# Performance work log

Measured on AMD Instinct MI355X. Metric: run time of the kernel, lower is better.

Reference implementation:

```python
import jax, jax.numpy as jnp
import numpy as np

N, D, H, L, E, G, C = 50000, 128, 128, 5, 800000, 512, 10


def setup_inputs() -> dict:
    key = jax.random.key(0)
    ks = jax.random.split(key, 16)
    s = 0.1  # normal init std (Weight_Initializer == 3 style; any init is fine for a math baseline)
    return {
        "x": jax.random.normal(ks[0], (N, D), jnp.float32),
        "edge_index": jax.random.randint(ks[1], (2, E), 0, N, jnp.int32),
        "edge_mask": jax.random.uniform(ks[2], (E,), jnp.float32),
        "batch": jnp.sort(jax.random.randint(ks[3], (N,), 0, G, jnp.int32)),
        "num_graphs": G,
        "eps": jnp.zeros((L,), jnp.float32),
        # per-GIN-layer 2-layer MLP (num_slp_layers=2): D -> H -> D, weights stored [in, out]
        "mlp_w1": jax.random.normal(ks[4], (L, D, H), jnp.float32) * s,
        "mlp_b1": jnp.zeros((L, H), jnp.float32),
        "mlp_w2": jax.random.normal(ks[5], (L, H, D), jnp.float32) * s,
        "mlp_b2": jnp.zeros((L, D), jnp.float32),
        # classifier head: lin1 [(L+1)*D -> (L+1)*D], lin2 [(L+1)*D -> C]
        "lin1_w": jax.random.normal(ks[6], ((L + 1) * D, (L + 1) * D), jnp.float32) * s,
        "lin1_b": jnp.zeros(((L + 1) * D,), jnp.float32),
        "lin2_w": jax.random.normal(ks[7], ((L + 1) * D, C), jnp.float32) * s,
        "lin2_b": jnp.zeros((C,), jnp.float32),
    }


def reference(x, edge_index, edge_mask, batch, num_graphs, eps,
              mlp_w1, mlp_b1, mlp_w2, mlp_b2, lin1_w, lin1_b, lin2_w, lin2_b):
    n = x.shape[0]
    src, dst = edge_index[0], edge_index[1]
    embeds = [x]
    h = x
    for l in range(eps.shape[0]):
        # A @ h with A[src,dst] = edge_mask: gather neighbor feats, weight, scatter-add to src
        agg = jax.ops.segment_sum(edge_mask[:, None] * h[dst], src, num_segments=n)  # [N,D]
        pooled = agg + (1.0 + eps[l]) * h
        h1 = jax.nn.relu(pooled @ mlp_w1[l] + mlp_b1[l])
        h = jax.nn.relu(h1 @ mlp_w2[l] + mlp_b2[l])
        embeds.append(h)
    stacked = jnp.stack(embeds)  # [L+1, N, D]
    # global_add_pool per layer, then per-graph concat across layers -> [G, (L+1)*D]
    pooled_g = jax.vmap(lambda e: jax.ops.segment_sum(e, batch, num_segments=num_graphs))(stacked)
    merged = jnp.transpose(pooled_g, (1, 0, 2)).reshape(num_graphs, -1)
    lin1_out = jax.nn.relu(merged @ lin1_w + lin1_b)  # dropout p=0 -> identity
    lin2_out = lin1_out @ lin2_w + lin2_b
    return jax.nn.softmax(lin2_out, axis=1)  # [G, C]
```

## Files before the change

### kernel.cpp

```cpp
#include <hip/hip_runtime.h>


typedef __bf16 bf16x8 __attribute__((ext_vector_type(8)));
typedef float f32x4 __attribute__((ext_vector_type(4)));

static inline int ceil_div(int a, int b) { return (a + b - 1) / b; }

__device__ inline ushort bf_rne(float v) {
  unsigned u = __float_as_uint(v);
  return (ushort)((u + 0x7fffu + ((u >> 16) & 1u)) >> 16);
}
__device__ inline float bf2f(ushort u) { return __uint_as_float((unsigned)u << 16); }
__device__ inline float bf2f_lo(unsigned g) { return __uint_as_float(g << 16); }
__device__ inline float bf2f_hi(unsigned g) { return __uint_as_float(g & 0xffff0000u); }

__global__ void k_hist(const int* __restrict__ src, int* __restrict__ deg, int E) {
  int i = blockIdx.x * blockDim.x + threadIdx.x;
  if (i < E) atomicAdd(&deg[src[i]], 1);
}

__global__ __launch_bounds__(256) void k_scan1(const int* __restrict__ deg,
                                               int* __restrict__ excl,
                                               int* __restrict__ bsum, int N) {
  __shared__ int tsum[256];
  int b = blockIdx.x, t = threadIdx.x;
  int base = b * 1024 + t * 4;
  int v0 = 0, v1 = 0, v2 = 0, v3 = 0;
  if (base + 3 < N) {
    int4 q = *(const int4*)&deg[base];
    v0 = q.x; v1 = q.y; v2 = q.z; v3 = q.w;
  } else {
    if (base + 0 < N) v0 = deg[base + 0];
    if (base + 1 < N) v1 = deg[base + 1];
    if (base + 2 < N) v2 = deg[base + 2];
    if (base + 3 < N) v3 = deg[base + 3];
  }
  tsum[t] = v0 + v1 + v2 + v3;
  __syncthreads();
  for (int off = 1; off < 256; off <<= 1) {
    int x = (t >= off) ? tsum[t - off] : 0;
    __syncthreads();
    tsum[t] += x;
    __syncthreads();
  }
  int pre = (t == 0) ? 0 : tsum[t - 1];
  if (base < N)     excl[base]     = pre;
  if (base + 1 < N) excl[base + 1] = pre + v0;
  if (base + 2 < N) excl[base + 2] = pre + v0 + v1;
  if (base + 3 < N) excl[base + 3] = pre + v0 + v1 + v2;
  if (t == 255) bsum[b] = tsum[255];
}

__global__ __launch_bounds__(256) void k_scan2(const int* __restrict__ bsum,
                                               int* __restrict__ boff, int nb,
                                               int* __restrict__ rowptr_last) {
  __shared__ int s[256];
  int t = threadIdx.x;
  s[t] = (t < nb) ? bsum[t] : 0;
  __syncthreads();
  for (int off = 1; off < 256; off <<= 1) {
    int x = (t >= off) ? s[t - off] : 0;
    __syncthreads();
    s[t] += x;
    __syncthreads();
  }
  if (t < nb) boff[t] = (t == 0) ? 0 : s[t - 1];
  if (t == 255) *rowptr_last = s[255];
}

__global__ __launch_bounds__(256) void k_scan3(const int* __restrict__ excl,
                                               const int* __restrict__ boff,
                                               int* __restrict__ rowptr,
                                               int* __restrict__ cursor, int N) {
  int i = blockIdx.x * 256 + threadIdx.x;
  if (i < N) {
    int v = excl[i] + boff[i >> 10];
    rowptr[i] = v;
    cursor[i] = v;
  }
}

__global__ void k_scatter(const int* __restrict__ src, const int* __restrict__ dst,
                          const float* __restrict__ mask, int* __restrict__ cursor,
                          int2* __restrict__ sedge, int E) {
  int i = blockIdx.x * blockDim.x + threadIdx.x;
  if (i < E) {
    int s = src[i];
    int p = atomicAdd(&cursor[s], 1);
    sedge[p] = make_int2(dst[i], __float_as_int(mask[i]));
  }
}

__global__ __launch_bounds__(256) void k_tobf16(const float* __restrict__ in,
                                                ushort* __restrict__ out, int n) {
  int base = (blockIdx.x * 256 + threadIdx.x) * 4;
  if (base + 3 < n) {
    float4 v = *(const float4*)&in[base];
    ushort4 o;
    o.x = bf_rne(v.x); o.y = bf_rne(v.y); o.z = bf_rne(v.z); o.w = bf_rne(v.w);
    *(ushort4*)&out[base] = o;
  } else {
    for (int k = base; k < n; ++k) out[k] = bf_rne(in[k]);
  }
}

__global__ __launch_bounds__(256) void k_prepw(const float* __restrict__ W,
                                               ushort* __restrict__ hi,
                                               ushort* __restrict__ lo,
                                               int K, int N) {
  __shared__ float t[32][33];
  int mat = blockIdx.z;
  const float* Wm = W + (size_t)mat * K * N;
  ushort* him = hi + (size_t)mat * K * N;
  ushort* lom = lo + (size_t)mat * K * N;
  int k0 = blockIdx.x * 32, n0 = blockIdx.y * 32;
  int tx = threadIdx.x & 31, ty = threadIdx.x >> 5;
#pragma unroll
  for (int r = 0; r < 32; r += 8)
    t[ty + r][tx] = Wm[(size_t)(k0 + ty + r) * N + n0 + tx];
  __syncthreads();
#pragma unroll
  for (int r = 0; r < 32; r += 8) {
    float v = t[tx][ty + r];
    size_t o = (size_t)(n0 + ty + r) * K + k0 + tx;
    ushort h = bf_rne(v);
    him[o] = h;
    lom[o] = bf_rne(v - bf2f(h));
  }
}

__global__ __launch_bounds__(128) void k_agg(const ushort* __restrict__ h,
                                             const int* __restrict__ rowptr,
                                             const int2* __restrict__ sedge,
                                             const float* __restrict__ eps, int layer,
                                             ushort* __restrict__ pooled, int N) {
  int v = blockIdx.x * 2 + (threadIdx.x >> 6);
  int lane = threadIdx.x & 63;
  if (v >= N) return;
  int beg = rowptr[v], end = rowptr[v + 1];
  float ax[8] = {}, ay[8] = {};
  int j = beg;
  for (; j + 8 <= end; j += 8) {
    int2 e[8];
    unsigned g[8];
#pragma unroll
    for (int q = 0; q < 8; ++q) e[q] = sedge[j + q];
#pragma unroll
    for (int q = 0; q < 8; ++q)
      g[q] = *(const unsigned*)&h[(size_t)e[q].x * 128 + lane * 2];
#pragma unroll
    for (int q = 0; q < 8; ++q) {
      float m = __int_as_float(e[q].y);
      ax[q] = fmaf(m, bf2f_lo(g[q]), ax[q]);
      ay[q] = fmaf(m, bf2f_hi(g[q]), ay[q]);
    }
  }
  for (; j + 2 <= end; j += 2) {
    int2 e0 = sedge[j], e1 = sedge[j + 1];
    unsigned g0 = *(const unsigned*)&h[(size_t)e0.x * 128 + lane * 2];
    unsigned g1 = *(const unsigned*)&h[(size_t)e1.x * 128 + lane * 2];
    ax[0] = fmaf(__int_as_float(e0.y), bf2f_lo(g0), ax[0]);
    ay[0] = fmaf(__int_as_float(e0.y), bf2f_hi(g0), ay[0]);
    ax[1] = fmaf(__int_as_float(e1.y), bf2f_lo(g1), ax[1]);
    ay[1] = fmaf(__int_as_float(e1.y), bf2f_hi(g1), ay[1]);
  }
  if (j < end) {
    int2 e = sedge[j];
    unsigned g = *(const unsigned*)&h[(size_t)e.x * 128 + lane * 2];
    float m = __int_as_float(e.y);
    ax[0] = fmaf(m, bf2f_lo(g), ax[0]);
    ay[0] = fmaf(m, bf2f_hi(g), ay[0]);
  }
  float sx = ((ax[0] + ax[1]) + (ax[2] + ax[3])) + ((ax[4] + ax[5]) + (ax[6] + ax[7]));
  float sy = ((ay[0] + ay[1]) + (ay[2] + ay[3])) + ((ay[4] + ay[5]) + (ay[6] + ay[7]));
  float ep = 1.0f + eps[layer];
  unsigned gs = *(const unsigned*)&h[(size_t)v * 128 + lane * 2];
  sx = fmaf(ep, bf2f_lo(gs), sx);
  sy = fmaf(ep, bf2f_hi(gs), sy);
  unsigned outw = (unsigned)bf_rne(sx) | ((unsigned)bf_rne(sy) << 16);
  *(unsigned*)&pooled[(size_t)v * 128 + lane * 2] = outw;
}

__global__ __launch_bounds__(256) void k_mlp(
    const ushort* __restrict__ pooled,
    const ushort* __restrict__ w1t, const float* __restrict__ b1,
    const ushort* __restrict__ w2t, const float* __restrict__ b2,
    ushort* __restrict__ hout, int N) {
  __shared__ ushort As[64][128];
  __shared__ ushort Ws[128][128];
  __shared__ ushort H1s[64][128];
  int tid = threadIdx.x;
  int w = tid >> 6, lane = tid & 63;
  int row0 = blockIdx.x * 64;
  int wr = w >> 1, wc = w & 1;

#pragma unroll
  for (int i = 0; i < 4; ++i) {
    int f = i * 256 + tid;
    int r = f >> 4, c8 = (f & 15) * 8;
    int ksw = c8 ^ ((r & 7) << 3);
    if (row0 + r < N) {
      *(bf16x8*)&As[r][ksw] = *(const bf16x8*)&pooled[(size_t)(row0 + r) * 128 + c8];
    } else {
      ushort4 z = {0, 0, 0, 0};
      *(ushort4*)&As[r][ksw] = z;
      *(ushort4*)&As[r][ksw + 4] = z;
    }
  }
#pragma unroll
  for (int i = 0; i < 8; ++i) {
    int f = i * 256 + tid;
    int r = f >> 4, c8 = (f & 15) * 8;
    *(bf16x8*)&Ws[r][c8 ^ ((r & 7) << 3)] = *(const bf16x8*)&w1t[(size_t)r * 128 + c8];
  }
  __syncthreads();

  f32x4 acc[2][4];
#pragma unroll
  for (int m = 0; m < 2; ++m)
#pragma unroll
    for (int n = 0; n < 4; ++n) acc[m][n] = (f32x4){0.f, 0.f, 0.f, 0.f};
#pragma unroll
  for (int ks = 0; ks < 4; ++ks) {
    int kk = ks * 32 + (lane >> 4) * 8;
    bf16x8 a[2], b[4];
#pragma unroll
    for (int m = 0; m < 2; ++m) {
      int r = wr * 32 + m * 16 + (lane & 15);
      a[m] = *(bf16x8*)&As[r][kk ^ ((r & 7) << 3)];
    }
#pragma unroll
    for (int n = 0; n < 4; ++n) {
      int r = wc * 64 + n * 16 + (lane & 15);
      b[n] = *(bf16x8*)&Ws[r][kk ^ ((r & 7) << 3)];
    }
#pragma unroll
    for (int m = 0; m < 2; ++m)
#pragma unroll
      for (int n = 0; n < 4; ++n)
        acc[m][n] = __builtin_amdgcn_mfma_f32_16x16x32_bf16(a[m], b[n], acc[m][n], 0, 0, 0);
  }
#pragma unroll
  for (int m = 0; m < 2; ++m) {
    int rbase = wr * 32 + m * 16 + (lane >> 4) * 4;
#pragma unroll
    for (int n = 0; n < 4; ++n) {
      int col = wc * 64 + n * 16 + (lane & 15);
      float bb = b1[col];
#pragma unroll
      for (int r = 0; r < 4; ++r) {
        int row = rbase + r;
        float v = fmaxf(acc[m][n][r] + bb, 0.f);
        H1s[row][col ^ ((row & 7) << 3)] = bf_rne(v);
      }
    }
  }
  __syncthreads();

#pragma unroll
  for (int i = 0; i < 8; ++i) {
    int f = i * 256 + tid;
    int r = f >> 4, c8 = (f & 15) * 8;
    *(bf16x8*)&Ws[r][c8 ^ ((r & 7) << 3)] = *(const bf16x8*)&w2t[(size_t)r * 128 + c8];
  }
  __syncthreads();

#pragma unroll
  for (int m = 0; m < 2; ++m)
#pragma unroll
    for (int n = 0; n < 4; ++n) acc[m][n] = (f32x4){0.f, 0.f, 0.f, 0.f};
#pragma unroll
  for (int ks = 0; ks < 4; ++ks) {
    int kk = ks * 32 + (lane >> 4) * 8;
    bf16x8 a[2], b[4];
#pragma unroll
    for (int m = 0; m < 2; ++m) {
      int r = wr * 32 + m * 16 + (lane & 15);
      a[m] = *(bf16x8*)&H1s[r][kk ^ ((r & 7) << 3)];
    }
#pragma unroll
    for (int n = 0; n < 4; ++n) {
      int r = wc * 64 + n * 16 + (lane & 15);
      b[n] = *(bf16x8*)&Ws[r][kk ^ ((r & 7) << 3)];
    }
#pragma unroll
    for (int m = 0; m < 2; ++m)
#pragma unroll
      for (int n = 0; n < 4; ++n)
        acc[m][n] = __builtin_amdgcn_mfma_f32_16x16x32_bf16(a[m], b[n], acc[m][n], 0, 0, 0);
  }
#pragma unroll
  for (int m = 0; m < 2; ++m) {
    int rbase = row0 + wr * 32 + m * 16 + (lane >> 4) * 4;
#pragma unroll
    for (int n = 0; n < 4; ++n) {
      int col = wc * 64 + n * 16 + (lane & 15);
      float bb = b2[col];
#pragma unroll
      for (int r = 0; r < 4; ++r) {
        int row = rbase + r;
        if (row < N) {
          float v = fmaxf(acc[m][n][r] + bb, 0.f);
          hout[(size_t)row * 128 + col] = bf_rne(v);
        }
      }
    }
  }
}

template <int RELU, int OUT_BF16, int SPLITW>
__global__ __launch_bounds__(256) void k_mgemm(const ushort* __restrict__ A,
                                               const ushort* __restrict__ Wt_hi,
                                               const ushort* __restrict__ Wt_lo,
                                               const float* __restrict__ bias,
                                               void* __restrict__ Cout,
                                               int M, int N, int K) {
  __shared__ ushort As[64][128];
  __shared__ ushort Ws_hi[64][128];
  __shared__ ushort Ws_lo[SPLITW ? 64 : 1][SPLITW ? 128 : 1];
  int tid = threadIdx.x;
  int row0 = blockIdx.y * 64, col0 = blockIdx.x * 64;
  int w = tid >> 6, lane = tid & 63;
  int wr = w >> 1, wc = w & 1;
  f32x4 acc[2][2] = {};
  int nk = K >> 7;
  for (int kc = 0; kc < nk; ++kc) {
    int k0 = kc << 7;
    if (kc) __syncthreads();
#pragma unroll
    for (int i = 0; i < 4; ++i) {
      int f = i * 256 + tid;
      int r = f >> 4, c8 = (f & 15) * 8;
      int ksw = c8 ^ ((r & 7) << 3);
      if (row0 + r < M) {
        *(bf16x8*)&As[r][ksw] = *(const bf16x8*)&A[(size_t)(row0 + r) * K + k0 + c8];
      } else {
        ushort4 z = {0, 0, 0, 0};
        *(ushort4*)&As[r][ksw] = z;
        *(ushort4*)&As[r][ksw + 4] = z;
      }
    }
#pragma unroll
    for (int i = 0; i < 4; ++i) {
      int f = i * 256 + tid;
      int r = f >> 4, c8 = (f & 15) * 8;
      int ksw = c8 ^ ((r & 7) << 3);
      *(bf16x8*)&Ws_hi[r][ksw] = *(const bf16x8*)&Wt_hi[(size_t)(col0 + r) * K + k0 + c8];
      if (SPLITW)
        *(bf16x8*)&Ws_lo[r][ksw] = *(const bf16x8*)&Wt_lo[(size_t)(col0 + r) * K + k0 + c8];
    }
    __syncthreads();
#pragma unroll
    for (int ks = 0; ks < 4; ++ks) {
      int kk = ks * 32 + (lane >> 4) * 8;
      bf16x8 a[2], bh[2], bl[2];
#pragma unroll
      for (int m = 0; m < 2; ++m) {
        int r = wr * 32 + m * 16 + (lane & 15);
        a[m] = *(bf16x8*)&As[r][kk ^ ((r & 7) << 3)];
      }
#pragma unroll
      for (int n = 0; n < 2; ++n) {
        int r = wc * 32 + n * 16 + (lane & 15);
        int ksw = kk ^ ((r & 7) << 3);
        bh[n] = *(bf16x8*)&Ws_hi[r][ksw];
        if (SPLITW) bl[n] = *(bf16x8*)&Ws_lo[r][ksw];
      }
#pragma unroll
      for (int m = 0; m < 2; ++m)
#pragma unroll
        for (int n = 0; n < 2; ++n) {
          acc[m][n] = __builtin_amdgcn_mfma_f32_16x16x32_bf16(a[m], bh[n], acc[m][n], 0, 0, 0);
          if (SPLITW)
            acc[m][n] = __builtin_amdgcn_mfma_f32_16x16x32_bf16(a[m], bl[n], acc[m][n], 0, 0, 0);
        }
    }
  }
#pragma unroll
  for (int m = 0; m < 2; ++m) {
    int rbase = row0 + wr * 32 + m * 16 + (lane >> 4) * 4;
#pragma unroll
    for (int n = 0; n < 2; ++n) {
      int col = col0 + wc * 32 + n * 16 + (lane & 15);
      float b = bias[col];
#pragma unroll
      for (int r = 0; r < 4; ++r) {
        int row = rbase + r;
        if (row < M) {
          float v = acc[m][n][r] + b;
          if (RELU) v = fmaxf(v, 0.f);
          if (OUT_BF16)
            ((ushort*)Cout)[(size_t)row * N + col] = bf_rne(v);
          else
            ((float*)Cout)[(size_t)row * N + col] = v;
        }
      }
    }
  }
}

__global__ __launch_bounds__(128) void k_pool_all(
    const ushort* __restrict__ f0, const ushort* __restrict__ f1,
    const ushort* __restrict__ f2, const ushort* __restrict__ f3,
    const ushort* __restrict__ f4, const ushort* __restrict__ f5,
    const int* __restrict__ batch, ushort* __restrict__ pg, int N, int L1) {
  __shared__ float red[2][64][2];
  int g = blockIdx.x;
  int slot = blockIdx.y;
  const ushort* feat;
  switch (slot) {
    case 0: feat = f0; break;
    case 1: feat = f1; break;
    case 2: feat = f2; break;
    case 3: feat = f3; break;
    case 4: feat = f4; break;
    default: feat = f5; break;
  }
  int w = threadIdx.x >> 6, lane = threadIdx.x & 63;
  int lo = 0, hi = N;
  while (lo < hi) {
    int mid = (lo + hi) >> 1;
    if (batch[mid] < g) lo = mid + 1; else hi = mid;
  }
  int s = lo;
  hi = N;
  while (lo < hi) {
    int mid = (lo + hi) >> 1;
    if (batch[mid] < g + 1) lo = mid + 1; else hi = mid;
  }
  int e = lo;
  float a0 = 0.f, a1 = 0.f;
#pragma unroll 4
  for (int v = s + w; v < e; v += 2) {
    unsigned u = *(const unsigned*)&feat[(size_t)v * 128 + lane * 2];
    a0 += bf2f_lo(u);
    a1 += bf2f_hi(u);
  }
  red[w][lane][0] = a0;
  red[w][lane][1] = a1;
  __syncthreads();
  if (w == 0) {
    a0 = red[0][lane][0] + red[1][lane][0];
    a1 = red[0][lane][1] + red[1][lane][1];
    unsigned outw = (unsigned)bf_rne(a0) | ((unsigned)bf_rne(a1) << 16);
    *(unsigned*)&pg[((size_t)g * L1 + slot) * 128 + lane * 2] = outw;
  }
}

__global__ __launch_bounds__(64) void k_lin2_softmax(const float* __restrict__ A,
                                                     const float* __restrict__ W,
                                                     const float* __restrict__ b,
                                                     float* __restrict__ out, int K, int C) {
  constexpr int CMAX = 16;
  int g = blockIdx.x;
  int lane = threadIdx.x;
  float acc[CMAX];
#pragma unroll
  for (int c = 0; c < CMAX; ++c) acc[c] = 0.f;
  for (int k = lane; k < K; k += 64) {
    float a = A[(size_t)g * K + k];
#pragma unroll
    for (int c = 0; c < CMAX; ++c)
      if (c < C) acc[c] = fmaf(a, W[(size_t)k * C + c], acc[c]);
  }
#pragma unroll
  for (int off = 32; off; off >>= 1)
#pragma unroll
    for (int c = 0; c < CMAX; ++c) acc[c] += __shfl_xor(acc[c], off, 64);
  if (lane == 0) {
    float mx = -3.0e38f;
#pragma unroll
    for (int c = 0; c < CMAX; ++c)
      if (c < C) {
        acc[c] += b[c];
        mx = fmaxf(mx, acc[c]);
      }
    float sum = 0.f;
#pragma unroll
    for (int c = 0; c < CMAX; ++c)
      if (c < C) {
        acc[c] = expf(acc[c] - mx);
        sum += acc[c];
      }
    float inv = 1.f / sum;
#pragma unroll
    for (int c = 0; c < CMAX; ++c)
      if (c < C) out[(size_t)g * C + c] = acc[c] * inv;
  }
}

extern "C" void kernel_launch(void* const* d_in, const int* in_sizes, int n_in,
                              void* d_out, int out_size, void* d_ws, size_t ws_size,
                              hipStream_t stream) {
  const float* x     = (const float*)d_in[0];
  const int*   eidx  = (const int*)d_in[1];
  const float* emask = (const float*)d_in[2];
  const int*   batch = (const int*)d_in[3];
  const float* eps   = (const float*)d_in[5];
  const float* w1    = (const float*)d_in[6];
  const float* b1    = (const float*)d_in[7];
  const float* w2    = (const float*)d_in[8];
  const float* b2    = (const float*)d_in[9];
  const float* l1w   = (const float*)d_in[10];
  const float* l1b   = (const float*)d_in[11];
  const float* l2w   = (const float*)d_in[12];
  const float* l2b   = (const float*)d_in[13];

  const int N = in_sizes[3];
  const int E = in_sizes[2];
  const int L = in_sizes[5];
  const int D = in_sizes[0] / N;
  const int C = in_sizes[13];
  const int G = out_size / C;
  const int L1 = L + 1;
  const int H = in_sizes[7] / L;
  const int F = L1 * D;

  const int* src = eidx;
  const int* dst = eidx + E;

  char* p = (char*)d_ws;
  auto carve = [&](size_t bytes) -> void* {
    void* r = (void*)p;
    p += (bytes + 255) & ~(size_t)255;
    return r;
  };
  int*    rowptr = (int*)carve((size_t)(N + 1) * 4);
  int*    cursor = (int*)carve((size_t)N * 4);
  int*    deg    = (int*)carve((size_t)N * 4);
  int*    excl   = (int*)carve((size_t)N * 4);
  int*    bsum   = (int*)carve(256 * 4);
  int*    boff   = (int*)carve(256 * 4);
  int2*   sedge  = (int2*)carve((size_t)E * 8);
  ushort* xb     = (ushort*)carve((size_t)N * D * 2);
  ushort* pooled = (ushort*)carve((size_t)N * D * 2);
  ushort* hb[5];
  for (int l = 0; l < 5; ++l) hb[l] = (ushort*)carve((size_t)N * D * 2);
  ushort* pg     = (ushort*)carve((size_t)G * F * 2);
  float*  l1out  = (float*)carve((size_t)G * F * 4);
  ushort* w1t_hi = (ushort*)carve((size_t)L * D * H * 2);
  ushort* w1t_lo = (ushort*)carve((size_t)L * D * H * 2);
  ushort* w2t_hi = (ushort*)carve((size_t)L * H * D * 2);
  ushort* w2t_lo = (ushort*)carve((size_t)L * H * D * 2);
  ushort* l1t_hi = (ushort*)carve((size_t)F * F * 2);
  ushort* l1t_lo = (ushort*)carve((size_t)F * F * 2);
  (void)ws_size;

  const int nb = ceil_div(N, 1024);
  hipMemsetAsync(deg, 0, (size_t)N * 4, stream);
  k_hist<<<ceil_div(E, 256), 256, 0, stream>>>(src, deg, E);
  k_scan1<<<nb, 256, 0, stream>>>(deg, excl, bsum, N);
  k_scan2<<<1, 256, 0, stream>>>(bsum, boff, nb, &rowptr[N]);
  k_scan3<<<ceil_div(N, 256), 256, 0, stream>>>(excl, boff, rowptr, cursor, N);
  k_scatter<<<ceil_div(E, 256), 256, 0, stream>>>(src, dst, emask, cursor, sedge, E);

  k_tobf16<<<ceil_div(N * D, 1024), 256, 0, stream>>>(x, xb, N * D);
  k_prepw<<<dim3(D / 32, H / 32, L), 256, 0, stream>>>(w1, w1t_hi, w1t_lo, D, H);
  k_prepw<<<dim3(H / 32, D / 32, L), 256, 0, stream>>>(w2, w2t_hi, w2t_lo, H, D);
  k_prepw<<<dim3(F / 32, F / 32, 1), 256, 0, stream>>>(l1w, l1t_hi, l1t_lo, F, F);

  const ushort* h_in = xb;
  for (int l = 0; l < L; ++l) {
    k_agg<<<ceil_div(N, 2), 128, 0, stream>>>(h_in, rowptr, sedge, eps, l, pooled, N);
    k_mlp<<<ceil_div(N, 64), 256, 0, stream>>>(
        pooled, w1t_hi + (size_t)l * D * H, b1 + (size_t)l * H,
        w2t_hi + (size_t)l * H * D, b2 + (size_t)l * D, hb[l], N);
    h_in = hb[l];
  }

  k_pool_all<<<dim3(G, L1), 128, 0, stream>>>(xb, hb[0], hb[1], hb[2], hb[3], hb[4],
                                              batch, pg, N, L1);

  k_mgemm<1, 0, 1><<<dim3(F / 64, ceil_div(G, 64)), 256, 0, stream>>>(
      pg, l1t_hi, l1t_lo, l1b, l1out, G, F, F);
  k_lin2_softmax<<<G, 64, 0, stream>>>(l1out, l2w, l2b, (float*)d_out, F, C);
}
```

Baseline: 428.5 us.

## Fuse global add pooling into MLP epilogue via shared-memory atomics

The MLP kernel's epilogue now accumulates per-graph sums into an fp32 pooled buffer. When a tile's nodes span at most 8 graphs it uses shared-memory atomics and then flushes to global, otherwise it falls back to direct global atomics. This removes the separate pooling pass that reread all six layer embeddings. Layer 0 is pooled from the fp32 input, the lin1 GEMM now converts the fp32 pooled input to bf16 on load, and the unused low-half weight conversion for the MLP weights is dropped. The cost is atomic traffic in the MLP epilogue, an extra memset, and a non-deterministic summation order.

```diff
diff --git a/kernel.cpp b/kernel.cpp
--- a/kernel.cpp
+++ b/kernel.cpp
@@ -104,15 +104,35 @@
   }
 }
 
+__global__ __launch_bounds__(256) void k_prepw12(const float* __restrict__ W1,
+                                                 const float* __restrict__ W2,
+                                                 ushort* __restrict__ hi1,
+                                                 ushort* __restrict__ hi2, int L) {
+  __shared__ float t[32][33];
+  int z = blockIdx.z;
+  const float* Wm = (z < L) ? (W1 + (size_t)z * 128 * 128)
+                            : (W2 + (size_t)(z - L) * 128 * 128);
+  ushort* him = (z < L) ? (hi1 + (size_t)z * 128 * 128)
+                        : (hi2 + (size_t)(z - L) * 128 * 128);
+  int k0 = blockIdx.x * 32, n0 = blockIdx.y * 32;
+  int tx = threadIdx.x & 31, ty = threadIdx.x >> 5;
+#pragma unroll
+  for (int r = 0; r < 32; r += 8)
+    t[ty + r][tx] = Wm[(size_t)(k0 + ty + r) * 128 + n0 + tx];
+  __syncthreads();
+#pragma unroll
+  for (int r = 0; r < 32; r += 8) {
+    float v = t[tx][ty + r];
+    him[(size_t)(n0 + ty + r) * 128 + k0 + tx] = bf_rne(v);
+  }
+}
+
 __global__ __launch_bounds__(256) void k_prepw(const float* __restrict__ W,
                                                ushort* __restrict__ hi,
                                                ushort* __restrict__ lo,
                                                int K, int N) {
   __shared__ float t[32][33];
-  int mat = blockIdx.z;
-  const float* Wm = W + (size_t)mat * K * N;
-  ushort* him = hi + (size_t)mat * K * N;
-  ushort* lom = lo + (size_t)mat * K * N;
+  const float* Wm = W;
   int k0 = blockIdx.x * 32, n0 = blockIdx.y * 32;
   int tx = threadIdx.x & 31, ty = threadIdx.x >> 5;
 #pragma unroll
@@ -124,8 +144,8 @@
     float v = t[tx][ty + r];
     size_t o = (size_t)(n0 + ty + r) * K + k0 + tx;
     ushort h = bf_rne(v);
-    him[o] = h;
-    lom[o] = bf_rne(v - bf2f(h));
+    hi[o] = h;
+    lo[o] = bf_rne(v - bf2f(h));
   }
 }
 
@@ -185,10 +205,13 @@
     const ushort* __restrict__ pooled,
     const ushort* __restrict__ w1t, const float* __restrict__ b1,
     const ushort* __restrict__ w2t, const float* __restrict__ b2,
-    ushort* __restrict__ hout, int N) {
+    ushort* __restrict__ hout, const int* __restrict__ batch,
+    float* __restrict__ pgf, int slotoff, int F, int N) {
   __shared__ ushort As[64][128];
   __shared__ ushort Ws[128][128];
   __shared__ ushort H1s[64][128];
+  float* pgpart = (float*)As;
+  int* bts = (int*)((char*)As + 4096);
   int tid = threadIdx.x;
   int w = tid >> 6, lane = tid & 63;
   int row0 = blockIdx.x * 64;
@@ -263,7 +286,16 @@
     int r = f >> 4, c8 = (f & 15) * 8;
     *(bf16x8*)&Ws[r][c8 ^ ((r & 7) << 3)] = *(const bf16x8*)&w2t[(size_t)r * 128 + c8];
   }
-  __syncthreads();
+  for (int idx = tid; idx < 1024; idx += 256) pgpart[idx] = 0.f;
+  if (tid < 64) {
+    int row = row0 + tid;
+    bts[tid] = batch[(row < N) ? row : (N - 1)];
+  }
+  __syncthreads();
+
+  int gmin = bts[0];
+  int span = bts[63] - gmin + 1;
+  bool fast = (span <= 8);
 
 #pragma unroll
   for (int m = 0; m < 2; ++m)
@@ -291,25 +323,40 @@
   }
 #pragma unroll
   for (int m = 0; m < 2; ++m) {
-    int rbase = row0 + wr * 32 + m * 16 + (lane >> 4) * 4;
+    int rlbase = wr * 32 + m * 16 + (lane >> 4) * 4;
 #pragma unroll
     for (int n = 0; n < 4; ++n) {
       int col = wc * 64 + n * 16 + (lane & 15);
       float bb = b2[col];
 #pragma unroll
       for (int r = 0; r < 4; ++r) {
-        int row = rbase + r;
+        int rl = rlbase + r;
+        int row = row0 + rl;
         if (row < N) {
           float v = fmaxf(acc[m][n][r] + bb, 0.f);
           hout[(size_t)row * 128 + col] = bf_rne(v);
+          int g = bts[rl];
+          if (fast)
+            atomicAdd(&pgpart[(g - gmin) * 128 + col], v);
+          else
+            atomicAdd(&pgf[(size_t)g * F + slotoff + col], v);
         }
       }
     }
   }
-}
-
-template <int RELU, int OUT_BF16, int SPLITW>
-__global__ __launch_bounds__(256) void k_mgemm(const ushort* __restrict__ A,
+  __syncthreads();
+  if (fast) {
+    int tot = span * 128;
+    for (int idx = tid; idx < tot; idx += 256) {
+      float v = pgpart[idx];
+      if (v != 0.f)
+        atomicAdd(&pgf[(size_t)(gmin + (idx >> 7)) * F + slotoff + (idx & 127)], v);
+    }
+  }
+}
+
+template <int RELU, int OUT_BF16, int SPLITW, int A_FP32>
+__global__ __launch_bounds__(256) void k_mgemm(const void* __restrict__ A,
                                                const ushort* __restrict__ Wt_hi,
                                                const ushort* __restrict__ Wt_lo,
                                                const float* __restrict__ bias,
@@ -333,7 +380,19 @@
       int r = f >> 4, c8 = (f & 15) * 8;
       int ksw = c8 ^ ((r & 7) << 3);
       if (row0 + r < M) {
-        *(bf16x8*)&As[r][ksw] = *(const bf16x8*)&A[(size_t)(row0 + r) * K + k0 + c8];
+        if (A_FP32) {
+          const float* Af = (const float*)A;
+          float4 v0 = *(const float4*)&Af[(size_t)(row0 + r) * K + k0 + c8];
+          float4 v1 = *(const float4*)&Af[(size_t)(row0 + r) * K + k0 + c8 + 4];
+          ushort4 h0, h1;
+          h0.x = bf_rne(v0.x); h0.y = bf_rne(v0.y); h0.z = bf_rne(v0.z); h0.w = bf_rne(v0.w);
+          h1.x = bf_rne(v1.x); h1.y = bf_rne(v1.y); h1.z = bf_rne(v1.z); h1.w = bf_rne(v1.w);
+          *(ushort4*)&As[r][ksw] = h0;
+          *(ushort4*)&As[r][ksw + 4] = h1;
+        } else {
+          const ushort* Ab = (const ushort*)A;
+          *(bf16x8*)&As[r][ksw] = *(const bf16x8*)&Ab[(size_t)(row0 + r) * K + k0 + c8];
+        }
       } else {
         ushort4 z = {0, 0, 0, 0};
         *(ushort4*)&As[r][ksw] = z;
@@ -399,24 +458,11 @@
   }
 }
 
-__global__ __launch_bounds__(128) void k_pool_all(
-    const ushort* __restrict__ f0, const ushort* __restrict__ f1,
-    const ushort* __restrict__ f2, const ushort* __restrict__ f3,
-    const ushort* __restrict__ f4, const ushort* __restrict__ f5,
-    const int* __restrict__ batch, ushort* __restrict__ pg, int N, int L1) {
-  __shared__ float red[2][64][2];
+__global__ __launch_bounds__(128) void k_pool0(const float* __restrict__ x,
+                                               const int* __restrict__ batch,
+                                               float* __restrict__ pgf, int N, int F) {
   int g = blockIdx.x;
-  int slot = blockIdx.y;
-  const ushort* feat;
-  switch (slot) {
-    case 0: feat = f0; break;
-    case 1: feat = f1; break;
-    case 2: feat = f2; break;
-    case 3: feat = f3; break;
-    case 4: feat = f4; break;
-    default: feat = f5; break;
-  }
-  int w = threadIdx.x >> 6, lane = threadIdx.x & 63;
+  int d = threadIdx.x;
   int lo = 0, hi = N;
   while (lo < hi) {
     int mid = (lo + hi) >> 1;
@@ -429,22 +475,9 @@
     if (batch[mid] < g + 1) lo = mid + 1; else hi = mid;
   }
   int e = lo;
-  float a0 = 0.f, a1 = 0.f;
-#pragma unroll 4
-  for (int v = s + w; v < e; v += 2) {
-    unsigned u = *(const unsigned*)&feat[(size_t)v * 128 + lane * 2];
-    a0 += bf2f_lo(u);
-    a1 += bf2f_hi(u);
-  }
-  red[w][lane][0] = a0;
-  red[w][lane][1] = a1;
-  __syncthreads();
-  if (w == 0) {
-    a0 = red[0][lane][0] + red[1][lane][0];
-    a1 = red[0][lane][1] + red[1][lane][1];
-    unsigned outw = (unsigned)bf_rne(a0) | ((unsigned)bf_rne(a1) << 16);
-    *(unsigned*)&pg[((size_t)g * L1 + slot) * 128 + lane * 2] = outw;
-  }
+  float acc = 0.f;
+  for (int v = s; v < e; ++v) acc += x[(size_t)v * 128 + d];
+  pgf[(size_t)g * F + d] = acc;
 }
 
 __global__ __launch_bounds__(64) void k_lin2_softmax(const float* __restrict__ A,
@@ -536,18 +569,17 @@
   ushort* pooled = (ushort*)carve((size_t)N * D * 2);
   ushort* hb[5];
   for (int l = 0; l < 5; ++l) hb[l] = (ushort*)carve((size_t)N * D * 2);
-  ushort* pg     = (ushort*)carve((size_t)G * F * 2);
+  float*  pgf    = (float*)carve((size_t)G * F * 4);
   float*  l1out  = (float*)carve((size_t)G * F * 4);
   ushort* w1t_hi = (ushort*)carve((size_t)L * D * H * 2);
-  ushort* w1t_lo = (ushort*)carve((size_t)L * D * H * 2);
   ushort* w2t_hi = (ushort*)carve((size_t)L * H * D * 2);
-  ushort* w2t_lo = (ushort*)carve((size_t)L * H * D * 2);
   ushort* l1t_hi = (ushort*)carve((size_t)F * F * 2);
   ushort* l1t_lo = (ushort*)carve((size_t)F * F * 2);
   (void)ws_size;
 
   const int nb = ceil_div(N, 1024);
   hipMemsetAsync(deg, 0, (size_t)N * 4, stream);
+  hipMemsetAsync(pgf, 0, (size_t)G * F * 4, stream);
   k_hist<<<ceil_div(E, 256), 256, 0, stream>>>(src, deg, E);
   k_scan1<<<nb, 256, 0, stream>>>(deg, excl, bsum, N);
   k_scan2<<<1, 256, 0, stream>>>(bsum, boff, nb, &rowptr[N]);
@@ -555,23 +587,22 @@
   k_scatter<<<ceil_div(E, 256), 256, 0, stream>>>(src, dst, emask, cursor, sedge, E);
 
   k_tobf16<<<ceil_div(N * D, 1024), 256, 0, stream>>>(x, xb, N * D);
-  k_prepw<<<dim3(D / 32, H / 32, L), 256, 0, stream>>>(w1, w1t_hi, w1t_lo, D, H);
-  k_prepw<<<dim3(H / 32, D / 32, L), 256, 0, stream>>>(w2, w2t_hi, w2t_lo, H, D);
-  k_prepw<<<dim3(F / 32, F / 32, 1), 256, 0, stream>>>(l1w, l1t_hi, l1t_lo, F, F);
+  k_prepw12<<<dim3(4, 4, 2 * L), 256, 0, stream>>>(w1, w2, w1t_hi, w2t_hi, L);
+  k_prepw<<<dim3(F / 32, F / 32), 256, 0, stream>>>(l1w, l1t_hi, l1t_lo, F, F);
+
+  k_pool0<<<G, 128, 0, stream>>>(x, batch, pgf, N, F);
 
   const ushort* h_in = xb;
   for (int l = 0; l < L; ++l) {
     k_agg<<<ceil_div(N, 2), 128, 0, stream>>>(h_in, rowptr, sedge, eps, l, pooled, N);
     k_mlp<<<ceil_div(N, 64), 256, 0, stream>>>(
         pooled, w1t_hi + (size_t)l * D * H, b1 + (size_t)l * H,
-        w2t_hi + (size_t)l * H * D, b2 + (size_t)l * D, hb[l], N);
+        w2t_hi + (size_t)l * H * D, b2 + (size_t)l * D, hb[l],
+        batch, pgf, (l + 1) * 128, F, N);
     h_in = hb[l];
   }
 
-  k_pool_all<<<dim3(G, L1), 128, 0, stream>>>(xb, hb[0], hb[1], hb[2], hb[3], hb[4],
-                                              batch, pg, N, L1);
-
-  k_mgemm<1, 0, 1><<<dim3(F / 64, ceil_div(G, 64)), 256, 0, stream>>>(
-      pg, l1t_hi, l1t_lo, l1b, l1out, G, F, F);
+  k_mgemm<1, 0, 1, 1><<<dim3(F / 64, ceil_div(G, 64)), 256, 0, stream>>>(
+      pgf, l1t_hi, l1t_lo, l1b, l1out, G, F, F);
   k_lin2_softmax<<<G, 64, 0, stream>>>(l1out, l2w, l2b, (float*)d_out, F, C);
 }
```

Result: slower. 636.9 us (+48.6%).
